# Kernel optimization log

Hardware: AMD Instinct MI355X
Metric: run time of the kernel (lower is better)

## Reference

```python
import jax, jax.numpy as jnp
import numpy as np

IN_DIM = 1024
LOW_D_FF = 128
OUT_DIM = 1024
B = 8
S = 2048

def _xavier_normal(key, shape):
    fan_in, fan_out = shape[1], shape[0]
    std = float(np.sqrt(2.0 / (fan_in + fan_out)))
    return jax.random.normal(key, shape, dtype=jnp.float32) * std

def setup_inputs() -> dict:
    key = jax.random.key(0)
    kx, kk, kd, ku = jax.random.split(key, 4)
    x = jax.random.normal(kx, (B, S, IN_DIM), dtype=jnp.float32)
    k = jax.random.normal(kk, (B, LOW_D_FF), dtype=jnp.float32)
    D_matrix = _xavier_normal(kd, (IN_DIM * LOW_D_FF, LOW_D_FF))
    U_matrix = _xavier_normal(ku, (LOW_D_FF * OUT_DIM, LOW_D_FF))
    return {"x": x, "k": k, "D_matrix": D_matrix, "U_matrix": U_matrix}

def reference(x, k, D_matrix, U_matrix):
    # x: [B, S, in_dim], k: [B, low_d_ff]
    Bn = x.shape[0]
    low = k.shape[-1]
    # hypernetwork weight generation: per-sample D [B, in_dim, low], U [B, low, out_dim]
    D = jnp.einsum('pk,bk->bp', D_matrix, k).reshape(Bn, IN_DIM, low)
    U = jnp.einsum('pk,bk->bp', U_matrix, k).reshape(Bn, low, OUT_DIM)
    h = jax.nn.relu(jnp.einsum('bsd,bdl->bsl', x, D))
    return jnp.einsum('bsl,blo->bso', h, U)
```

## Files before the change

### kernel.cpp

```cpp
#include <hip/hip_runtime.h>
#include <hip/hip_bf16.h>
#include <stdint.h>

#define IN_DIM  1024
#define LOW     128
#define OUT_DIM 1024
#define BATCH   8
#define SEQ     2048

typedef unsigned short u16;
typedef short bf16x8 __attribute__((ext_vector_type(8)));
typedef unsigned short u16x4 __attribute__((ext_vector_type(4)));
typedef float f32x4 __attribute__((ext_vector_type(4)));

__device__ __forceinline__ u16 f2bf(float f) {
    union { float f; uint32_t u; } v;
    v.f = f;
    uint32_t u = v.u;
    return (u16)((u + 0x7fffu + ((u >> 16) & 1u)) >> 16);
}

__global__ __launch_bounds__(256) void gen_w(const float* __restrict__ Dm,
                                             const float* __restrict__ Um,
                                             const float* __restrict__ kv,
                                             u16* __restrict__ DgT,
                                             u16* __restrict__ UgT) {
    __shared__ float stage[16 * 128];
    __shared__ u16 tb[BATCH * 8 * 32];

    int t = threadIdx.x;
    int bid = blockIdx.x;
    bool isU = bid >= 512;
    int rb = isU ? (bid - 512) : bid;
    const float* src = isU ? Um : Dm;
    u16* out = isU ? UgT : DgT;
    int NTOT = isU ? 1024 : 128;
    int MTOT = isU ? 128 : 1024;
    int sh = isU ? 7 : 4;
    int m0 = (rb >> sh) * 32;
    int n0 = (rb & ((1 << sh) - 1)) * 8;

    int r  = t >> 4;
    int bp = (t >> 2) & 3;
    int q  = t & 3;
    int sw = ((q << 1) ^ (r & 7)) & 7;

    f32x4 kr0[8], kr1[8];
#pragma unroll
    for (int j4 = 0; j4 < 8; ++j4) {
        kr0[j4] = *(const f32x4*)(kv + (2 * bp)     * LOW + q * 32 + j4 * 4);
        kr1[j4] = *(const f32x4*)(kv + (2 * bp + 1) * LOW + q * 32 + j4 * 4);
    }

    for (int ch = 0; ch < 16; ++ch) {
        __syncthreads();
#pragma unroll
        for (int i = 0; i < 2; ++i) {
            int f = t + 256 * i;
            int rs = f >> 5, c = f & 31;
            int qs = c >> 3, j4s = c & 7;
            int cp = (qs << 3) | (j4s ^ (((qs << 1) ^ (rs & 7)) & 7));
            int m = m0 + 2 * ch + (rs >> 3);
            int n = n0 + (rs & 7);
            f32x4 v = *(const f32x4*)(src + ((size_t)m * NTOT + n) * 128 + c * 4);
            *(f32x4*)(stage + rs * 128 + cp * 4) = v;
        }
        __syncthreads();
        float a0 = 0.f, a1 = 0.f;
#pragma unroll
        for (int j4 = 0; j4 < 8; ++j4) {
            f32x4 a = *(const f32x4*)(stage + r * 128 + ((q << 3) | (j4 ^ sw)) * 4);
            a0 += a.x * kr0[j4].x + a.y * kr0[j4].y + a.z * kr0[j4].z + a.w * kr0[j4].w;
            a1 += a.x * kr1[j4].x + a.y * kr1[j4].y + a.z * kr1[j4].z + a.w * kr1[j4].w;
        }
        a0 += __shfl_xor(a0, 1); a0 += __shfl_xor(a0, 2);
        a1 += __shfl_xor(a1, 1); a1 += __shfl_xor(a1, 2);
        if (q == 0) {
            int nn = r & 7, mm = 2 * ch + (r >> 3);
            tb[(2 * bp)     * 256 + nn * 32 + mm] = f2bf(a0);
            tb[(2 * bp + 1) * 256 + nn * 32 + mm] = f2bf(a1);
        }
    }
    __syncthreads();
    int c64 = t >> 2, q4 = t & 3;
    int bw = c64 >> 3, np = c64 & 7;
    bf16x8 v = *(const bf16x8*)(tb + bw * 256 + np * 32 + q4 * 8);
    *(bf16x8*)(out + ((size_t)(bw * NTOT + n0 + np)) * MTOT + m0 + q4 * 8) = v;
}

__global__ __launch_bounds__(256) void fc1(const float* __restrict__ x,
                                           const u16* __restrict__ DgT,
                                           u16* __restrict__ h) {
    __shared__ u16 As[32][72];
    __shared__ u16 Bs[128][72];
    int t = threadIdx.x;
    int bid = blockIdx.x;
    int b = bid >> 6, st = bid & 63;
    int s0 = st * 32;
    const float* xb = x + ((size_t)b * SEQ + s0) * IN_DIM;
    const u16* Db = DgT + (size_t)b * LOW * IN_DIM;

    int w = t >> 6, lane = t & 63;
    int wm = w >> 1, wn = w & 1;
    int lr = lane & 15, hi = lane >> 4;

    f32x4 acc[4];
#pragma unroll
    for (int nf = 0; nf < 4; ++nf) acc[nf] = (f32x4){0.f, 0.f, 0.f, 0.f};

    int ar = t >> 3, ac = t & 7;
    int brt = t >> 3, bc = t & 7;

    for (int kt = 0; kt < IN_DIM / 64; ++kt) {
        int k0 = kt * 64;
#pragma unroll
        for (int i = 0; i < 2; ++i) {
            float4 v = *(const float4*)(xb + (size_t)ar * IN_DIM + k0 + ac * 4 + i * 32);
            u16x4 o;
            o.x = f2bf(v.x); o.y = f2bf(v.y); o.z = f2bf(v.z); o.w = f2bf(v.w);
            *(u16x4*)(&As[ar][ac * 4 + i * 32]) = o;
        }
#pragma unroll
        for (int i = 0; i < 4; ++i) {
            int row = brt + 32 * i;
            bf16x8 v = *(const bf16x8*)(Db + (size_t)row * IN_DIM + k0 + bc * 8);
            *(bf16x8*)(&Bs[row][bc * 8]) = v;
        }
        __syncthreads();
#pragma unroll
        for (int ks = 0; ks < 2; ++ks) {
            int kk = ks * 32 + hi * 8;
            bf16x8 af = *(const bf16x8*)(&As[wm * 16 + lr][kk]);
#pragma unroll
            for (int nf = 0; nf < 4; ++nf) {
                bf16x8 bf = *(const bf16x8*)(&Bs[wn * 64 + nf * 16 + lr][kk]);
                acc[nf] = __builtin_amdgcn_mfma_f32_16x16x32_bf16(af, bf, acc[nf], 0, 0, 0);
            }
        }
        __syncthreads();
    }
    u16* hb = h + ((size_t)b * SEQ + s0) * LOW;
#pragma unroll
    for (int nf = 0; nf < 4; ++nf) {
        int col = wn * 64 + nf * 16 + lr;
#pragma unroll
        for (int j = 0; j < 4; ++j) {
            int rrow = wm * 16 + hi * 4 + j;
            hb[(size_t)rrow * LOW + col] = f2bf(fmaxf(acc[nf][j], 0.f));
        }
    }
}

__global__ __launch_bounds__(256) void fc2(const u16* __restrict__ h,
                                           const u16* __restrict__ UgT,
                                           float* __restrict__ out) {
    __shared__ u16 As[128 * 128];
    __shared__ u16 Bs[128 * 128];
    int t = threadIdx.x;
    int bid = blockIdx.x;
    int b = bid >> 7, st = (bid >> 3) & 15, ot = bid & 7;
    int s0 = st * 128, o0 = ot * 128;
    const u16* hb = h + ((size_t)b * SEQ + s0) * LOW;
    const u16* Ub = UgT + ((size_t)b * OUT_DIM + o0) * LOW;

#pragma unroll
    for (int i = 0; i < 8; ++i) {
        int ch = i * 256 + t;
        int row = ch >> 4, c = ch & 15;
        int swc = c ^ (row & 7);
        *(bf16x8*)(As + row * 128 + swc * 8) = *(const bf16x8*)(hb + (size_t)ch * 8);
        *(bf16x8*)(Bs + row * 128 + swc * 8) = *(const bf16x8*)(Ub + (size_t)ch * 8);
    }
    __syncthreads();

    int w = t >> 6, lane = t & 63;
    int wm = w >> 1, wn = w & 1;
    int lr = lane & 15, lkc = (lane >> 4);

    f32x4 acc[4][4];
#pragma unroll
    for (int mf = 0; mf < 4; ++mf)
#pragma unroll
        for (int nf = 0; nf < 4; ++nf)
            acc[mf][nf] = (f32x4){0.f, 0.f, 0.f, 0.f};

#pragma unroll
    for (int ks = 0; ks < 4; ++ks) {
        bf16x8 af[4], bfr[4];
#pragma unroll
        for (int mf = 0; mf < 4; ++mf) {
            int row = wm * 64 + mf * 16 + lr;
            int swc = (ks * 4 + lkc) ^ (row & 7);
            af[mf] = *(const bf16x8*)(As + row * 128 + swc * 8);
        }
#pragma unroll
        for (int nf = 0; nf < 4; ++nf) {
            int row = wn * 64 + nf * 16 + lr;
            int swc = (ks * 4 + lkc) ^ (row & 7);
            bfr[nf] = *(const bf16x8*)(Bs + row * 128 + swc * 8);
        }
#pragma unroll
        for (int mf = 0; mf < 4; ++mf)
#pragma unroll
            for (int nf = 0; nf < 4; ++nf)
                acc[mf][nf] = __builtin_amdgcn_mfma_f32_16x16x32_bf16(
                    af[mf], bfr[nf], acc[mf][nf], 0, 0, 0);
    }

    float* ob = out + ((size_t)b * SEQ + s0) * OUT_DIM + o0;
#pragma unroll
    for (int mf = 0; mf < 4; ++mf)
#pragma unroll
        for (int nf = 0; nf < 4; ++nf) {
            int col = wn * 64 + nf * 16 + lr;
#pragma unroll
            for (int j = 0; j < 4; ++j) {
                int rrow = wm * 64 + mf * 16 + (lane >> 4) * 4 + j;
                ob[(size_t)rrow * OUT_DIM + col] = acc[mf][nf][j];
            }
        }
}

extern "C" void kernel_launch(void* const* d_in, const int* in_sizes, int n_in,
                              void* d_out, int out_size, void* d_ws, size_t ws_size,
                              hipStream_t stream) {
    const float* x  = (const float*)d_in[0];
    const float* kv = (const float*)d_in[1];
    const float* Dm = (const float*)d_in[2];
    const float* Um = (const float*)d_in[3];
    float* out = (float*)d_out;

    u16* DgT = (u16*)d_ws;
    u16* UgT = DgT + (size_t)BATCH * LOW * IN_DIM;
    u16* hbuf = UgT + (size_t)BATCH * OUT_DIM * LOW;

    gen_w<<<dim3(1024), dim3(256), 0, stream>>>(Dm, Um, kv, DgT, UgT);
    fc1<<<dim3(512), dim3(256), 0, stream>>>(x, DgT, hbuf);
    fc2<<<dim3(1024), dim3(256), 0, stream>>>(hbuf, UgT, out);
}
```

Before: 71.56 us.

## Use MFMA with register double-buffered loads in hypernetwork weight generation

The weight-generation kernel drops its LDS-staged FP32 dot products and 16-step synchronized loop. Each wave now loads the D/U matrix rows straight into registers, converts them to bf16, and multiplies by a bf16 fragment of k with MFMA instructions, padding the batch dimension from 8 to 16. Loads for the next tile are issued before the current tile is computed, using two register buffers. This removes the per-chunk barriers and the scalar FMA work, but it rounds the generation inputs to bf16, which lowers accuracy, and it wastes half of each MFMA on padding.

```diff
diff --git a/kernel.cpp b/kernel.cpp
--- a/kernel.cpp
+++ b/kernel.cpp
@@ -25,67 +25,89 @@
                                              const float* __restrict__ kv,
                                              u16* __restrict__ DgT,
                                              u16* __restrict__ UgT) {
-    __shared__ float stage[16 * 128];
-    __shared__ u16 tb[BATCH * 8 * 32];
+    __shared__ u16 tb[8 * 8 * 32];
 
     int t = threadIdx.x;
     int bid = blockIdx.x;
     bool isU = bid >= 512;
     int rb = isU ? (bid - 512) : bid;
     const float* src = isU ? Um : Dm;
-    u16* out = isU ? UgT : DgT;
+    u16* outp = isU ? UgT : DgT;
     int NTOT = isU ? 1024 : 128;
     int MTOT = isU ? 128 : 1024;
     int sh = isU ? 7 : 4;
     int m0 = (rb >> sh) * 32;
     int n0 = (rb & ((1 << sh) - 1)) * 8;
 
-    int r  = t >> 4;
-    int bp = (t >> 2) & 3;
-    int q  = t & 3;
-    int sw = ((q << 1) ^ (r & 7)) & 7;
-
-    f32x4 kr0[8], kr1[8];
-#pragma unroll
-    for (int j4 = 0; j4 < 8; ++j4) {
-        kr0[j4] = *(const f32x4*)(kv + (2 * bp)     * LOW + q * 32 + j4 * 4);
-        kr1[j4] = *(const f32x4*)(kv + (2 * bp + 1) * LOW + q * 32 + j4 * 4);
-    }
-
-    for (int ch = 0; ch < 16; ++ch) {
-        __syncthreads();
-#pragma unroll
-        for (int i = 0; i < 2; ++i) {
-            int f = t + 256 * i;
-            int rs = f >> 5, c = f & 31;
-            int qs = c >> 3, j4s = c & 7;
-            int cp = (qs << 3) | (j4s ^ (((qs << 1) ^ (rs & 7)) & 7));
-            int m = m0 + 2 * ch + (rs >> 3);
-            int n = n0 + (rs & 7);
-            f32x4 v = *(const f32x4*)(src + ((size_t)m * NTOT + n) * 128 + c * 4);
-            *(f32x4*)(stage + rs * 128 + cp * 4) = v;
-        }
-        __syncthreads();
-        float a0 = 0.f, a1 = 0.f;
-#pragma unroll
-        for (int j4 = 0; j4 < 8; ++j4) {
-            f32x4 a = *(const f32x4*)(stage + r * 128 + ((q << 3) | (j4 ^ sw)) * 4);
-            a0 += a.x * kr0[j4].x + a.y * kr0[j4].y + a.z * kr0[j4].z + a.w * kr0[j4].w;
-            a1 += a.x * kr1[j4].x + a.y * kr1[j4].y + a.z * kr1[j4].z + a.w * kr1[j4].w;
-        }
-        a0 += __shfl_xor(a0, 1); a0 += __shfl_xor(a0, 2);
-        a1 += __shfl_xor(a1, 1); a1 += __shfl_xor(a1, 2);
-        if (q == 0) {
-            int nn = r & 7, mm = 2 * ch + (r >> 3);
-            tb[(2 * bp)     * 256 + nn * 32 + mm] = f2bf(a0);
-            tb[(2 * bp + 1) * 256 + nn * 32 + mm] = f2bf(a1);
-        }
-    }
+    int lane = t & 63, w = t >> 6;
+    int lr = lane & 15;
+    int hi = lane >> 4;
+
+    bf16x8 bfrag[4];
+#pragma unroll
+    for (int ks = 0; ks < 4; ++ks)
+#pragma unroll
+        for (int j = 0; j < 8; ++j) {
+            float kvf = (lr < 8) ? kv[lr * LOW + ks * 32 + hi * 8 + j] : 0.f;
+            bfrag[ks][j] = (short)f2bf(kvf);
+        }
+
+    const float* abase = src +
+        ((size_t)(m0 + w * 8 + (lr >> 3)) * NTOT + n0 + (lr & 7)) * 128 + hi * 8;
+    size_t tstep = (size_t)2 * NTOT * 128;
+
+#define ISSUE(Lb, tau)                                                        \
+    {                                                                         \
+        const float* rp = abase + (size_t)(tau) * tstep;                      \
+        _Pragma("unroll")                                                     \
+        for (int ks = 0; ks < 4; ++ks) {                                      \
+            Lb[2 * ks]     = *(const f32x4*)(rp + ks * 32);                   \
+            Lb[2 * ks + 1] = *(const f32x4*)(rp + ks * 32 + 4);               \
+        }                                                                     \
+    }
+
+#define COMPUTE(Lb, tau)                                                      \
+    {                                                                         \
+        f32x4 acc = (f32x4){0.f, 0.f, 0.f, 0.f};                              \
+        _Pragma("unroll")                                                     \
+        for (int ks = 0; ks < 4; ++ks) {                                      \
+            f32x4 v0 = Lb[2 * ks], v1 = Lb[2 * ks + 1];                       \
+            bf16x8 afr;                                                       \
+            afr[0] = (short)f2bf(v0.x); afr[1] = (short)f2bf(v0.y);           \
+            afr[2] = (short)f2bf(v0.z); afr[3] = (short)f2bf(v0.w);           \
+            afr[4] = (short)f2bf(v1.x); afr[5] = (short)f2bf(v1.y);           \
+            afr[6] = (short)f2bf(v1.z); afr[7] = (short)f2bf(v1.w);           \
+            acc = __builtin_amdgcn_mfma_f32_16x16x32_bf16(afr, bfrag[ks],     \
+                                                          acc, 0, 0, 0);      \
+        }                                                                     \
+        if (lr < 8) {                                                         \
+            _Pragma("unroll")                                                 \
+            for (int j = 0; j < 4; ++j) {                                     \
+                int r = hi * 4 + j;                                           \
+                int mm = w * 8 + (tau) * 2 + (r >> 3);                        \
+                tb[lr * 256 + (r & 7) * 32 + mm] = f2bf(acc[j]);              \
+            }                                                                 \
+        }                                                                     \
+    }
+
+    f32x4 LA[8], LB[8];
+    ISSUE(LA, 0)
+    ISSUE(LB, 1)
+    COMPUTE(LA, 0)
+    ISSUE(LA, 2)
+    COMPUTE(LB, 1)
+    ISSUE(LB, 3)
+    COMPUTE(LA, 2)
+    COMPUTE(LB, 3)
+#undef ISSUE
+#undef COMPUTE
+
     __syncthreads();
+
     int c64 = t >> 2, q4 = t & 3;
     int bw = c64 >> 3, np = c64 & 7;
     bf16x8 v = *(const bf16x8*)(tb + bw * 256 + np * 32 + q4 * 8);
-    *(bf16x8*)(out + ((size_t)(bw * NTOT + n0 + np)) * MTOT + m0 + q4 * 8) = v;
+    *(bf16x8*)(outp + ((size_t)(bw * NTOT + n0 + np)) * MTOT + m0 + q4 * 8) = v;
 }
 
 __global__ __launch_bounds__(256) void fc1(const float* __restrict__ x,
```

Result: faster. 69.51 us (-2.9%).
